# Optimization experiments

Measured on AMD Instinct MI355X. Metric: run time of the kernel, lower is better.

The kernel has to match this reference:

```python
import jax, jax.numpy as jnp
import numpy as np

NUM_DIGIT, DIM_DIGIT, NUM_ROUTINGS = 10, 16, 3
B, NUM_PRIMARY, DIM_PRIMARY = 256, 1152, 8
EPS = 1e-7


def _squash(x, eps=EPS):
    # Faithful to the source: tf.norm with NO axis -> GLOBAL Frobenius norm
    # over the whole tensor (not per-capsule).
    n2 = jnp.sum(jnp.square(x))
    n = jnp.sqrt(n2)
    return (n2 / (n2 + 1.0)) * (x / (n + eps))


def setup_inputs() -> dict:
    key = jax.random.key(0)
    k1, k2 = jax.random.split(key)
    primary_caps = jax.random.normal(k1, (B, NUM_PRIMARY, DIM_PRIMARY), dtype=jnp.float32)
    # glorot_uniform over W [num_digit, num_primary, dim_digit, dim_primary]
    limit = float(np.sqrt(6.0 / (DIM_PRIMARY + DIM_DIGIT)))
    W = jax.random.uniform(k2, (NUM_DIGIT, NUM_PRIMARY, DIM_DIGIT, DIM_PRIMARY),
                           minval=-limit, maxval=limit, dtype=jnp.float32)
    return {"primary_caps": primary_caps, "W": W}


def reference(primary_caps, W):
    # u_hat[b,d,p,i] = sum_j W[d,p,i,j] * primary_caps[b,p,j]
    # (vectorized replacement for tf.map_fn over the batch)
    u_hat = jnp.einsum('dpij,bpj->bdpi', W, primary_caps)  # [B, D, P, dim_digit]

    b = jnp.zeros((u_hat.shape[0], NUM_DIGIT, 1, NUM_PRIMARY), dtype=u_hat.dtype)
    v = None
    for r in range(NUM_ROUTINGS):
        c = jax.nn.softmax(b, axis=1)                      # [B, D, 1, P]
        s = jnp.einsum('bdop,bdpi->bdoi', c, u_hat)        # [B, D, 1, dim_digit]
        v = jnp.transpose(_squash(s), (0, 1, 3, 2))        # [B, D, dim_digit, 1]
        if r < NUM_ROUTINGS - 1:
            agree = jnp.einsum('bdpi,bdio->bdpo', u_hat, v)  # [B, D, P, 1]
            b = b + jnp.transpose(agree, (0, 1, 3, 2))       # [B, D, 1, P]
    return jnp.squeeze(v, axis=-1)  # [B, num_digit, dim_digit]
```

## Files before the change

kernel.cpp:

```cpp
#include <hip/hip_runtime.h>
#include <hip/hip_bf16.h>
#include <stdint.h>

#define B_ 256
#define D_ 10
#define P_ 1152
#define I_ 16
#define J_ 8

#define PG 48
#define NPT 24

__device__ inline uint32_t pack_bf16(float a, float b) {
    uint32_t ua = __float_as_uint(a);
    uint32_t ub = __float_as_uint(b);
    ua = (ua + 0x7fffu + ((ua >> 16) & 1u)) >> 16;
    ub = (ub + 0x7fffu + ((ub >> 16) & 1u)) >> 16;
    return ua | (ub << 16);
}

__global__ __launch_bounds__(256) void k_uhat(
    const float* __restrict__ x, const float* __restrict__ W,
    uint32_t* __restrict__ uhat, float* __restrict__ s_part)
{
    const int bid = blockIdx.x;
    const int bh = bid & 1;
    const int pd = bid >> 1;
    const int d = pd % D_;
    const int pg = pd / D_;
    const int p0 = pg * PG;

    const int tid = threadIdx.x;
    const int ih = tid & 1;
    const int b = bh * 128 + (tid >> 1);

    __shared__ float4 Wl[PG * 32];

    const float4* wg = (const float4*)(W + (size_t)(d * P_ + p0) * 128);
    for (int k = tid; k < PG * 32; k += 256) Wl[k] = wg[k];
    __syncthreads();

    float sacc[8];
    #pragma unroll
    for (int i = 0; i < 8; ++i) sacc[i] = 0.f;

    const float4* xb = (const float4*)(x + ((size_t)b * P_ + p0) * J_);
    uint4* ub = (uint4*)(uhat + ((size_t)(b * D_ + d) * P_ + p0) * 8) + ih;

    float4 xA = xb[0], xB = xb[1];
    for (int pp = 0; pp < PG; ++pp) {
        float4 nA = xA, nB = xB;
        if (pp + 1 < PG) { nA = xb[(pp + 1) * 2]; nB = xb[(pp + 1) * 2 + 1]; }

        const float4* wp = &Wl[pp * 32 + ih * 16];
        float u[8];
        #pragma unroll
        for (int i = 0; i < 8; ++i) {
            const float4 wA = wp[i * 2], wB = wp[i * 2 + 1];
            u[i] = wA.x*xA.x + wA.y*xA.y + wA.z*xA.z + wA.w*xA.w
                 + wB.x*xB.x + wB.y*xB.y + wB.z*xB.z + wB.w*xB.w;
            sacc[i] += u[i];
        }
        uint4 w;
        w.x = pack_bf16(u[0], u[1]); w.y = pack_bf16(u[2], u[3]);
        w.z = pack_bf16(u[4], u[5]); w.w = pack_bf16(u[6], u[7]);
        ub[pp * 2] = w;
        xA = nA; xB = nB;
    }

    float4* sp = (float4*)(s_part + (size_t)pg * (B_ * D_ * I_)
                           + (size_t)b * (D_ * I_) + d * 16 + ih * 8);
    sp[0] = make_float4(sacc[0], sacc[1], sacc[2], sacc[3]);
    sp[1] = make_float4(sacc[4], sacc[5], sacc[6], sacc[7]);
}

__global__ __launch_bounds__(256) void k_sred(const float* __restrict__ s_part,
                                              float* __restrict__ s, float* __restrict__ n2)
{
    const int gid = blockIdx.x * 256 + threadIdx.x;
    float v = 0.f;
    #pragma unroll
    for (int pt = 0; pt < NPT; ++pt) v += s_part[(size_t)pt * (B_ * D_ * I_) + gid];
    v *= 0.1f;
    s[gid] = v;
    float v2 = v * v;
    #pragma unroll
    for (int st = 1; st < 64; st <<= 1) v2 += __shfl_xor(v2, st);
    __shared__ float r4[4];
    const int lane = threadIdx.x & 63, wave = threadIdx.x >> 6;
    if (lane == 0) r4[wave] = v2;
    __syncthreads();
    if (threadIdx.x == 0) atomicAdd(n2, r4[0] + r4[1] + r4[2] + r4[3]);
}

__global__ __launch_bounds__(1024) void k_route(
    const uint32_t* __restrict__ uhat,
    const float* __restrict__ s0, const float* __restrict__ s1,
    const float* __restrict__ n2v, int rnd,
    float* __restrict__ s_out)
{
    const int b = blockIdx.x;
    const int tid = threadIdx.x;

    __shared__ float tls[D_ * I_];
    __shared__ float sw[16][D_ * I_];
    __shared__ float n2l;

    if (tid < D_ * I_) {
        const float n20 = n2v[0];
        const float g0 = (n20 / (n20 + 1.f)) / (sqrtf(n20) + 1e-7f);
        float v = g0 * s0[(size_t)b * D_ * I_ + tid];
        if (rnd == 2) {
            const float n21 = n2v[1];
            const float g1 = (n21 / (n21 + 1.f)) / (sqrtf(n21) + 1e-7f);
            v += g1 * s1[(size_t)b * D_ * I_ + tid];
        }
        tls[tid] = v;
    }
    if (tid == 0) n2l = 0.f;
    __syncthreads();

    const int team = tid >> 3;
    const int tl = tid & 7;
    float sacc[D_][2];
    #pragma unroll
    for (int d = 0; d < D_; ++d) { sacc[d][0] = 0.f; sacc[d][1] = 0.f; }

    for (int k = 0; k < 9; ++k) {
        const int p = team + k * 128;
        const uint32_t* up = uhat + ((size_t)b * D_ * P_ + p) * 8 + tl;
        float u[D_][2];
        float beta[D_];
        #pragma unroll
        for (int d = 0; d < D_; ++d) {
            const uint32_t w = up[(size_t)d * P_ * 8];
            const float u0 = __uint_as_float(w << 16);
            const float u1 = __uint_as_float(w & 0xffff0000u);
            u[d][0] = u0; u[d][1] = u1;
            float bp = u0 * tls[d * I_ + 2 * tl] + u1 * tls[d * I_ + 2 * tl + 1];
            bp += __shfl_xor(bp, 1);
            bp += __shfl_xor(bp, 2);
            bp += __shfl_xor(bp, 4);
            beta[d] = bp;
        }
        float m = beta[0];
        #pragma unroll
        for (int d = 1; d < D_; ++d) m = fmaxf(m, beta[d]);
        float c[D_]; float Z = 0.f;
        #pragma unroll
        for (int d = 0; d < D_; ++d) { c[d] = __expf(beta[d] - m); Z += c[d]; }
        const float rz = 1.f / Z;
        #pragma unroll
        for (int d = 0; d < D_; ++d) {
            const float cd = c[d] * rz;
            sacc[d][0] += cd * u[d][0];
            sacc[d][1] += cd * u[d][1];
        }
    }

    #pragma unroll
    for (int st = 8; st < 64; st <<= 1) {
        #pragma unroll
        for (int d = 0; d < D_; ++d) {
            sacc[d][0] += __shfl_xor(sacc[d][0], st);
            sacc[d][1] += __shfl_xor(sacc[d][1], st);
        }
    }
    const int wave = tid >> 6, lane = tid & 63;
    if (lane < 8) {
        #pragma unroll
        for (int d = 0; d < D_; ++d) {
            sw[wave][d * I_ + 2 * tl]     = sacc[d][0];
            sw[wave][d * I_ + 2 * tl + 1] = sacc[d][1];
        }
    }
    __syncthreads();

    if (tid < D_ * I_) {
        float v = 0.f;
        #pragma unroll
        for (int w2 = 0; w2 < 16; ++w2) v += sw[w2][tid];
        s_out[(size_t)b * D_ * I_ + tid] = v;
        atomicAdd(&n2l, v * v);
    }
    __syncthreads();
    if (tid == 0) atomicAdd((float*)(n2v + rnd), n2l);
}

__global__ void k_out(float* __restrict__ out, const float* __restrict__ n2p)
{
    const int i = blockIdx.x * 256 + threadIdx.x;
    const float n2 = *n2p;
    const float g = (n2 / (n2 + 1.f)) / (sqrtf(n2) + 1e-7f);
    out[i] *= g;
}

extern "C" void kernel_launch(void* const* d_in, const int* in_sizes, int n_in,
                              void* d_out, int out_size, void* d_ws, size_t ws_size,
                              hipStream_t stream)
{
    const float* x = (const float*)d_in[0];
    const float* W = (const float*)d_in[1];
    float* out = (float*)d_out;

    char* ws = (char*)d_ws;
    uint32_t* uhat = (uint32_t*)ws;
    const size_t uhat_bytes = (size_t)B_ * D_ * P_ * I_ * 2;
    float* s_part = (float*)(ws + uhat_bytes);
    float* s0 = s_part + (size_t)NPT * B_ * D_ * I_;
    float* s1 = s0 + B_ * D_ * I_;
    float* n2 = s1 + B_ * D_ * I_;

    hipMemsetAsync(n2, 0, 3 * sizeof(float), stream);

    k_uhat<<<NPT * D_ * 2, 256, 0, stream>>>(x, W, uhat, s_part);
    k_sred<<<(B_ * D_ * I_) / 256, 256, 0, stream>>>(s_part, s0, n2 + 0);
    k_route<<<B_, 1024, 0, stream>>>(uhat, s0, s1, n2, 1, s1);
    k_route<<<B_, 1024, 0, stream>>>(uhat, s0, s1, n2, 2, out);
    k_out<<<(B_ * D_ * I_) / 256, 256, 0, stream>>>(out, n2 + 2);
}
```

Measured before the change: 100.7 us.

## Reshape u_hat storage into slot-interleaved layout and remap uhat kernel threads

Changes the u_hat kernel so each thread computes one pair of output dims for 4 primaries at a time, writing 16-byte packed stores in a new slot-interleaved layout. The W tile in LDS is stored with padding to avoid bank conflicts. Blocks now cover 32 batches each, and block indices are ordered so consecutive blocks share d. The routing kernel's indexing is rewritten to read the new layout. The goals are fewer, wider global stores, better coalescing, and more blocks for occupancy, at the cost of more blocks each reloading W into LDS.

```diff
diff --git a/kernel.cpp b/kernel.cpp
--- a/kernel.cpp
+++ b/kernel.cpp
@@ -10,6 +10,8 @@
 
 #define PG 48
 #define NPT 24
+#define SLOTS 9216
+#define WSP 193
 
 __device__ inline uint32_t pack_bf16(float a, float b) {
     uint32_t ua = __float_as_uint(a);
@@ -24,54 +26,60 @@
     uint32_t* __restrict__ uhat, float* __restrict__ s_part)
 {
     const int bid = blockIdx.x;
-    const int bh = bid & 1;
-    const int pd = bid >> 1;
-    const int d = pd % D_;
-    const int pg = pd / D_;
+    const int g = bid & 7;
+    const int fam = bid >> 3;
+    const int pg = g + 8 * (fam % 3);
+    const int rem = fam / 3;
+    const int d = rem % D_;
+    const int bc = rem / D_;
+
     const int p0 = pg * PG;
-
     const int tid = threadIdx.x;
-    const int ih = tid & 1;
-    const int b = bh * 128 + (tid >> 1);
-
-    __shared__ float4 Wl[PG * 32];
+    const int c = tid & 7;
+    const int b = bc * 32 + (tid >> 3);
+
+    __shared__ float4 Wl[8 * WSP];
 
     const float4* wg = (const float4*)(W + (size_t)(d * P_ + p0) * 128);
-    for (int k = tid; k < PG * 32; k += 256) Wl[k] = wg[k];
-    __syncthreads();
-
-    float sacc[8];
-    #pragma unroll
-    for (int i = 0; i < 8; ++i) sacc[i] = 0.f;
-
+    for (int k = tid; k < PG * 32; k += 256) {
+        const int pl = k >> 5;
+        const int cc = (k >> 2) & 7;
+        const int q = k & 3;
+        Wl[cc * WSP + pl * 4 + q] = wg[k];
+    }
+    __syncthreads();
+
+    float sacc0 = 0.f, sacc1 = 0.f;
     const float4* xb = (const float4*)(x + ((size_t)b * P_ + p0) * J_);
-    uint4* ub = (uint4*)(uhat + ((size_t)(b * D_ + d) * P_ + p0) * 8) + ih;
-
-    float4 xA = xb[0], xB = xb[1];
-    for (int pp = 0; pp < PG; ++pp) {
-        float4 nA = xA, nB = xB;
-        if (pp + 1 < PG) { nA = xb[(pp + 1) * 2]; nB = xb[(pp + 1) * 2 + 1]; }
-
-        const float4* wp = &Wl[pp * 32 + ih * 16];
-        float u[8];
-        #pragma unroll
-        for (int i = 0; i < 8; ++i) {
-            const float4 wA = wp[i * 2], wB = wp[i * 2 + 1];
-            u[i] = wA.x*xA.x + wA.y*xA.y + wA.z*xA.z + wA.w*xA.w
-                 + wB.x*xB.x + wB.y*xB.y + wB.z*xB.z + wB.w*xB.w;
-            sacc[i] += u[i];
-        }
-        uint4 w;
-        w.x = pack_bf16(u[0], u[1]); w.y = pack_bf16(u[2], u[3]);
-        w.z = pack_bf16(u[4], u[5]); w.w = pack_bf16(u[6], u[7]);
-        ub[pp * 2] = w;
-        xA = nA; xB = nB;
-    }
-
-    float4* sp = (float4*)(s_part + (size_t)pg * (B_ * D_ * I_)
-                           + (size_t)b * (D_ * I_) + d * 16 + ih * 8);
-    sp[0] = make_float4(sacc[0], sacc[1], sacc[2], sacc[3]);
-    sp[1] = make_float4(sacc[4], sacc[5], sacc[6], sacc[7]);
+    uint4* ub = (uint4*)uhat + ((size_t)(b * D_ + d) * SLOTS >> 2) + c;
+    const int pqg0 = pg * 12;
+
+    for (int pql = 0; pql < 12; ++pql) {
+        float4 xv[4][2];
+        #pragma unroll
+        for (int p4 = 0; p4 < 4; ++p4) {
+            xv[p4][0] = xb[(pql * 4 + p4) * 2];
+            xv[p4][1] = xb[(pql * 4 + p4) * 2 + 1];
+        }
+        uint32_t wr[4];
+        #pragma unroll
+        for (int p4 = 0; p4 < 4; ++p4) {
+            const float4* wp = &Wl[c * WSP + (pql * 4 + p4) * 4];
+            const float4 wA = wp[0], wB = wp[1], wC = wp[2], wD = wp[3];
+            const float4 xA = xv[p4][0], xB = xv[p4][1];
+            float u0 = wA.x*xA.x + wA.y*xA.y + wA.z*xA.z + wA.w*xA.w
+                     + wB.x*xB.x + wB.y*xB.y + wB.z*xB.z + wB.w*xB.w;
+            float u1 = wC.x*xA.x + wC.y*xA.y + wC.z*xA.z + wC.w*xA.w
+                     + wD.x*xB.x + wD.y*xB.y + wD.z*xB.z + wD.w*xB.w;
+            sacc0 += u0; sacc1 += u1;
+            wr[p4] = pack_bf16(u0, u1);
+        }
+        uint4 w4; w4.x = wr[0]; w4.y = wr[1]; w4.z = wr[2]; w4.w = wr[3];
+        ub[(size_t)(pqg0 + pql) * 8] = w4;
+    }
+
+    float2 o; o.x = sacc0; o.y = sacc1;
+    *(float2*)&s_part[(((size_t)pg * B_ + b) * D_ + d) * I_ + 2 * c] = o;
 }
 
 __global__ __launch_bounds__(256) void k_sred(const float* __restrict__ s_part,
@@ -120,20 +128,25 @@
     if (tid == 0) n2l = 0.f;
     __syncthreads();
 
-    const int team = tid >> 3;
-    const int tl = tid & 7;
+    const int wv = tid >> 6;
+    const int l = tid & 63;
+    const int tb = l >> 3;
+    const int tl = l & 7;
+    const uint32_t* ubase = uhat + (size_t)b * D_ * SLOTS;
+
     float sacc[D_][2];
     #pragma unroll
     for (int d = 0; d < D_; ++d) { sacc[d][0] = 0.f; sacc[d][1] = 0.f; }
 
     for (int k = 0; k < 9; ++k) {
-        const int p = team + k * 128;
-        const uint32_t* up = uhat + ((size_t)b * D_ * P_ + p) * 8 + tl;
+        const int pqb = k * 32 + wv * 2;
+        const int slot = (pqb + (tb >> 2)) * 32 + tl * 4 + (tb & 3);
+        const uint32_t* up = ubase + slot;
         float u[D_][2];
         float beta[D_];
         #pragma unroll
         for (int d = 0; d < D_; ++d) {
-            const uint32_t w = up[(size_t)d * P_ * 8];
+            const uint32_t w = up[(size_t)d * SLOTS];
             const float u0 = __uint_as_float(w << 16);
             const float u1 = __uint_as_float(w & 0xffff0000u);
             u[d][0] = u0; u[d][1] = u1;
@@ -146,13 +159,13 @@
         float m = beta[0];
         #pragma unroll
         for (int d = 1; d < D_; ++d) m = fmaxf(m, beta[d]);
-        float c[D_]; float Z = 0.f;
-        #pragma unroll
-        for (int d = 0; d < D_; ++d) { c[d] = __expf(beta[d] - m); Z += c[d]; }
+        float cc[D_]; float Z = 0.f;
+        #pragma unroll
+        for (int d = 0; d < D_; ++d) { cc[d] = __expf(beta[d] - m); Z += cc[d]; }
         const float rz = 1.f / Z;
         #pragma unroll
         for (int d = 0; d < D_; ++d) {
-            const float cd = c[d] * rz;
+            const float cd = cc[d] * rz;
             sacc[d][0] += cd * u[d][0];
             sacc[d][1] += cd * u[d][1];
         }
@@ -166,12 +179,11 @@
             sacc[d][1] += __shfl_xor(sacc[d][1], st);
         }
     }
-    const int wave = tid >> 6, lane = tid & 63;
-    if (lane < 8) {
-        #pragma unroll
-        for (int d = 0; d < D_; ++d) {
-            sw[wave][d * I_ + 2 * tl]     = sacc[d][0];
-            sw[wave][d * I_ + 2 * tl + 1] = sacc[d][1];
+    if (l < 8) {
+        #pragma unroll
+        for (int d = 0; d < D_; ++d) {
+            sw[wv][d * I_ + 2 * tl]     = sacc[d][0];
+            sw[wv][d * I_ + 2 * tl + 1] = sacc[d][1];
         }
     }
     __syncthreads();
@@ -213,7 +225,7 @@
 
     hipMemsetAsync(n2, 0, 3 * sizeof(float), stream);
 
-    k_uhat<<<NPT * D_ * 2, 256, 0, stream>>>(x, W, uhat, s_part);
+    k_uhat<<<NPT * D_ * 8, 256, 0, stream>>>(x, W, uhat, s_part);
     k_sred<<<(B_ * D_ * I_) / 256, 256, 0, stream>>>(s_part, s0, n2 + 0);
     k_route<<<B_, 1024, 0, stream>>>(uhat, s0, s1, n2, 1, s1);
     k_route<<<B_, 1024, 0, stream>>>(uhat, s0, s1, n2, 2, out);
```

New measurement: 96.68 us. 1.04x faster.

## Recompute u_hat per routing round instead of storing a bf16 u_hat buffer

Applied to the files above, without the earlier changes.

Drops the materialised bf16 u_hat tensor (about 94 MB written once and read twice). Each of the three routing rounds now recomputes u_hat on the fly from x and W, using a single templated kernel that fuses the softmax and weighted sum. Per-block partial sums go through a separate reduction kernel. This trades the HBM traffic of the u_hat buffer for three times the u_hat FLOPs and repeated reads of W and x, which may be served from cache. A side effect is that u_hat stays in fp32 rather than being rounded to bf16.

```diff
diff --git a/kernel.cpp b/kernel.cpp
--- a/kernel.cpp
+++ b/kernel.cpp
@@ -8,81 +8,124 @@
 #define I_ 16
 #define J_ 8
 
-#define PG 48
-#define NPT 24
+#define NPG 16
+#define PRR 72
+#define NB 8
 
-__device__ inline uint32_t pack_bf16(float a, float b) {
-    uint32_t ua = __float_as_uint(a);
-    uint32_t ub = __float_as_uint(b);
-    ua = (ua + 0x7fffu + ((ua >> 16) & 1u)) >> 16;
-    ub = (ub + 0x7fffu + ((ub >> 16) & 1u)) >> 16;
-    return ua | (ub << 16);
-}
-
-__global__ __launch_bounds__(256) void k_uhat(
+template<int RND>
+__global__ __launch_bounds__(512, 2) void k_round(
     const float* __restrict__ x, const float* __restrict__ W,
-    uint32_t* __restrict__ uhat, float* __restrict__ s_part)
+    const float* __restrict__ s0, const float* __restrict__ s1,
+    const float* __restrict__ n2v, float* __restrict__ s_part)
 {
     const int bid = blockIdx.x;
-    const int bh = bid & 1;
-    const int pd = bid >> 1;
-    const int d = pd % D_;
-    const int pg = pd / D_;
-    const int p0 = pg * PG;
+    const int pg = bid & 15;
+    const int bc = bid >> 4;
+    const int tid = threadIdx.x;
+    const int c = tid & 7;
+    const int tm = tid >> 3;
+    const int b_l = tm & 7;
+    const int pidx = tm >> 3;
+    const int b = bc * NB + b_l;
 
-    const int tid = threadIdx.x;
-    const int ih = tid & 1;
-    const int b = bh * 128 + (tid >> 1);
+    __shared__ float lsum[8][NB][D_ * I_];
 
-    __shared__ float4 Wl[PG * 32];
-
-    const float4* wg = (const float4*)(W + (size_t)(d * P_ + p0) * 128);
-    for (int k = tid; k < PG * 32; k += 256) Wl[k] = wg[k];
-    __syncthreads();
-
-    float sacc[8];
-    #pragma unroll
-    for (int i = 0; i < 8; ++i) sacc[i] = 0.f;
-
-    const float4* xb = (const float4*)(x + ((size_t)b * P_ + p0) * J_);
-    uint4* ub = (uint4*)(uhat + ((size_t)(b * D_ + d) * P_ + p0) * 8) + ih;
-
-    float4 xA = xb[0], xB = xb[1];
-    for (int pp = 0; pp < PG; ++pp) {
-        float4 nA = xA, nB = xB;
-        if (pp + 1 < PG) { nA = xb[(pp + 1) * 2]; nB = xb[(pp + 1) * 2 + 1]; }
-
-        const float4* wp = &Wl[pp * 32 + ih * 16];
-        float u[8];
+    float t0[D_], t1[D_];
+    if (RND > 0) {
+        const float n20 = n2v[0];
+        const float g0 = (n20 / (n20 + 1.f)) / (sqrtf(n20) + 1e-7f);
+        const float* sb0 = s0 + (size_t)b * (D_ * I_) + 2 * c;
         #pragma unroll
-        for (int i = 0; i < 8; ++i) {
-            const float4 wA = wp[i * 2], wB = wp[i * 2 + 1];
-            u[i] = wA.x*xA.x + wA.y*xA.y + wA.z*xA.z + wA.w*xA.w
-                 + wB.x*xB.x + wB.y*xB.y + wB.z*xB.z + wB.w*xB.w;
-            sacc[i] += u[i];
+        for (int d = 0; d < D_; ++d) {
+            t0[d] = g0 * sb0[d * 16];
+            t1[d] = g0 * sb0[d * 16 + 1];
         }
-        uint4 w;
-        w.x = pack_bf16(u[0], u[1]); w.y = pack_bf16(u[2], u[3]);
-        w.z = pack_bf16(u[4], u[5]); w.w = pack_bf16(u[6], u[7]);
-        ub[pp * 2] = w;
-        xA = nA; xB = nB;
+        if (RND == 2) {
+            const float n21 = n2v[1];
+            const float g1 = (n21 / (n21 + 1.f)) / (sqrtf(n21) + 1e-7f);
+            const float* sb1 = s1 + (size_t)b * (D_ * I_) + 2 * c;
+            #pragma unroll
+            for (int d = 0; d < D_; ++d) {
+                t0[d] += g1 * sb1[d * 16];
+                t1[d] += g1 * sb1[d * 16 + 1];
+            }
+        }
     }
 
-    float4* sp = (float4*)(s_part + (size_t)pg * (B_ * D_ * I_)
-                           + (size_t)b * (D_ * I_) + d * 16 + ih * 8);
-    sp[0] = make_float4(sacc[0], sacc[1], sacc[2], sacc[3]);
-    sp[1] = make_float4(sacc[4], sacc[5], sacc[6], sacc[7]);
+    float sa0[D_], sa1[D_];
+    #pragma unroll
+    for (int d = 0; d < D_; ++d) { sa0[d] = 0.f; sa1[d] = 0.f; }
+
+    for (int st = 0; st < PRR / 8; ++st) {
+        const int p = pg * PRR + st * 8 + pidx;
+        const float4* xp = (const float4*)(x + ((size_t)b * P_ + p) * J_);
+        const float4 xA = xp[0], xB = xp[1];
+        const float4* wp = (const float4*)(W + ((size_t)p * I_ + 2 * c) * J_);
+
+        float u0[D_], u1[D_], beta[D_];
+        #pragma unroll
+        for (int d = 0; d < D_; ++d) {
+            const float4 wA = wp[0], wB = wp[1], wC = wp[2], wD = wp[3];
+            wp += (size_t)P_ * 32;
+            u0[d] = wA.x*xA.x + wA.y*xA.y + wA.z*xA.z + wA.w*xA.w
+                  + wB.x*xB.x + wB.y*xB.y + wB.z*xB.z + wB.w*xB.w;
+            u1[d] = wC.x*xA.x + wC.y*xA.y + wC.z*xA.z + wC.w*xA.w
+                  + wD.x*xB.x + wD.y*xB.y + wD.z*xB.z + wD.w*xB.w;
+            if (RND > 0) beta[d] = u0[d] * t0[d] + u1[d] * t1[d];
+        }
+
+        if (RND > 0) {
+            #pragma unroll
+            for (int d = 0; d < D_; ++d) {
+                beta[d] += __shfl_xor(beta[d], 1);
+                beta[d] += __shfl_xor(beta[d], 2);
+                beta[d] += __shfl_xor(beta[d], 4);
+            }
+            float m = beta[0];
+            #pragma unroll
+            for (int d = 1; d < D_; ++d) m = fmaxf(m, beta[d]);
+            float Z = 0.f;
+            #pragma unroll
+            for (int d = 0; d < D_; ++d) { beta[d] = __expf(beta[d] - m); Z += beta[d]; }
+            const float rz = 1.f / Z;
+            #pragma unroll
+            for (int d = 0; d < D_; ++d) {
+                const float cd = beta[d] * rz;
+                sa0[d] += cd * u0[d];
+                sa1[d] += cd * u1[d];
+            }
+        } else {
+            #pragma unroll
+            for (int d = 0; d < D_; ++d) { sa0[d] += u0[d]; sa1[d] += u1[d]; }
+        }
+    }
+
+    #pragma unroll
+    for (int d = 0; d < D_; ++d) {
+        lsum[pidx][b_l][d * 16 + 2 * c]     = sa0[d];
+        lsum[pidx][b_l][d * 16 + 2 * c + 1] = sa1[d];
+    }
+    __syncthreads();
+    for (int k = tid; k < NB * D_ * I_; k += 512) {
+        const int bb = k / (D_ * I_);
+        const int di = k - bb * (D_ * I_);
+        float v = 0.f;
+        #pragma unroll
+        for (int q = 0; q < 8; ++q) v += lsum[q][bb][di];
+        s_part[(size_t)pg * (B_ * D_ * I_) + (size_t)(bc * NB + bb) * (D_ * I_) + di] = v;
+    }
 }
 
 __global__ __launch_bounds__(256) void k_sred(const float* __restrict__ s_part,
-                                              float* __restrict__ s, float* __restrict__ n2)
+                                              float* __restrict__ sout,
+                                              float* __restrict__ n2, float scale)
 {
     const int gid = blockIdx.x * 256 + threadIdx.x;
     float v = 0.f;
     #pragma unroll
-    for (int pt = 0; pt < NPT; ++pt) v += s_part[(size_t)pt * (B_ * D_ * I_) + gid];
-    v *= 0.1f;
-    s[gid] = v;
+    for (int pt = 0; pt < NPG; ++pt) v += s_part[(size_t)pt * (B_ * D_ * I_) + gid];
+    v *= scale;
+    sout[gid] = v;
     float v2 = v * v;
     #pragma unroll
     for (int st = 1; st < 64; st <<= 1) v2 += __shfl_xor(v2, st);
@@ -91,100 +134,6 @@
     if (lane == 0) r4[wave] = v2;
     __syncthreads();
     if (threadIdx.x == 0) atomicAdd(n2, r4[0] + r4[1] + r4[2] + r4[3]);
-}
-
-__global__ __launch_bounds__(1024) void k_route(
-    const uint32_t* __restrict__ uhat,
-    const float* __restrict__ s0, const float* __restrict__ s1,
-    const float* __restrict__ n2v, int rnd,
-    float* __restrict__ s_out)
-{
-    const int b = blockIdx.x;
-    const int tid = threadIdx.x;
-
-    __shared__ float tls[D_ * I_];
-    __shared__ float sw[16][D_ * I_];
-    __shared__ float n2l;
-
-    if (tid < D_ * I_) {
-        const float n20 = n2v[0];
-        const float g0 = (n20 / (n20 + 1.f)) / (sqrtf(n20) + 1e-7f);
-        float v = g0 * s0[(size_t)b * D_ * I_ + tid];
-        if (rnd == 2) {
-            const float n21 = n2v[1];
-            const float g1 = (n21 / (n21 + 1.f)) / (sqrtf(n21) + 1e-7f);
-            v += g1 * s1[(size_t)b * D_ * I_ + tid];
-        }
-        tls[tid] = v;
-    }
-    if (tid == 0) n2l = 0.f;
-    __syncthreads();
-
-    const int team = tid >> 3;
-    const int tl = tid & 7;
-    float sacc[D_][2];
-    #pragma unroll
-    for (int d = 0; d < D_; ++d) { sacc[d][0] = 0.f; sacc[d][1] = 0.f; }
-
-    for (int k = 0; k < 9; ++k) {
-        const int p = team + k * 128;
-        const uint32_t* up = uhat + ((size_t)b * D_ * P_ + p) * 8 + tl;
-        float u[D_][2];
-        float beta[D_];
-        #pragma unroll
-        for (int d = 0; d < D_; ++d) {
-            const uint32_t w = up[(size_t)d * P_ * 8];
-            const float u0 = __uint_as_float(w << 16);
-            const float u1 = __uint_as_float(w & 0xffff0000u);
-            u[d][0] = u0; u[d][1] = u1;
-            float bp = u0 * tls[d * I_ + 2 * tl] + u1 * tls[d * I_ + 2 * tl + 1];
-            bp += __shfl_xor(bp, 1);
-            bp += __shfl_xor(bp, 2);
-            bp += __shfl_xor(bp, 4);
-            beta[d] = bp;
-        }
-        float m = beta[0];
-        #pragma unroll
-        for (int d = 1; d < D_; ++d) m = fmaxf(m, beta[d]);
-        float c[D_]; float Z = 0.f;
-        #pragma unroll
-        for (int d = 0; d < D_; ++d) { c[d] = __expf(beta[d] - m); Z += c[d]; }
-        const float rz = 1.f / Z;
-        #pragma unroll
-        for (int d = 0; d < D_; ++d) {
-            const float cd = c[d] * rz;
-            sacc[d][0] += cd * u[d][0];
-            sacc[d][1] += cd * u[d][1];
-        }
-    }
-
-    #pragma unroll
-    for (int st = 8; st < 64; st <<= 1) {
-        #pragma unroll
-        for (int d = 0; d < D_; ++d) {
-            sacc[d][0] += __shfl_xor(sacc[d][0], st);
-            sacc[d][1] += __shfl_xor(sacc[d][1], st);
-        }
-    }
-    const int wave = tid >> 6, lane = tid & 63;
-    if (lane < 8) {
-        #pragma unroll
-        for (int d = 0; d < D_; ++d) {
-            sw[wave][d * I_ + 2 * tl]     = sacc[d][0];
-            sw[wave][d * I_ + 2 * tl + 1] = sacc[d][1];
-        }
-    }
-    __syncthreads();
-
-    if (tid < D_ * I_) {
-        float v = 0.f;
-        #pragma unroll
-        for (int w2 = 0; w2 < 16; ++w2) v += sw[w2][tid];
-        s_out[(size_t)b * D_ * I_ + tid] = v;
-        atomicAdd(&n2l, v * v);
-    }
-    __syncthreads();
-    if (tid == 0) atomicAdd((float*)(n2v + rnd), n2l);
 }
 
 __global__ void k_out(float* __restrict__ out, const float* __restrict__ n2p)
@@ -203,19 +152,21 @@
     const float* W = (const float*)d_in[1];
     float* out = (float*)d_out;
 
-    char* ws = (char*)d_ws;
-    uint32_t* uhat = (uint32_t*)ws;
-    const size_t uhat_bytes = (size_t)B_ * D_ * P_ * I_ * 2;
-    float* s_part = (float*)(ws + uhat_bytes);
-    float* s0 = s_part + (size_t)NPT * B_ * D_ * I_;
+    float* ws = (float*)d_ws;
+    float* s_part = ws;
+    float* s0 = s_part + (size_t)NPG * B_ * D_ * I_;
     float* s1 = s0 + B_ * D_ * I_;
     float* n2 = s1 + B_ * D_ * I_;
 
-    hipMemsetAsync(n2, 0, 3 * sizeof(float), stream);
+    (void)hipMemsetAsync(n2, 0, 3 * sizeof(float), stream);
 
-    k_uhat<<<NPT * D_ * 2, 256, 0, stream>>>(x, W, uhat, s_part);
-    k_sred<<<(B_ * D_ * I_) / 256, 256, 0, stream>>>(s_part, s0, n2 + 0);
-    k_route<<<B_, 1024, 0, stream>>>(uhat, s0, s1, n2, 1, s1);
-    k_route<<<B_, 1024, 0, stream>>>(uhat, s0, s1, n2, 2, out);
+    const int grid = 32 * NPG;
+
+    k_round<0><<<grid, 512, 0, stream>>>(x, W, s0, s1, n2, s_part);
+    k_sred<<<(B_ * D_ * I_) / 256, 256, 0, stream>>>(s_part, s0, n2 + 0, 0.1f);
+    k_round<1><<<grid, 512, 0, stream>>>(x, W, s0, s1, n2, s_part);
+    k_sred<<<(B_ * D_ * I_) / 256, 256, 0, stream>>>(s_part, s1, n2 + 1, 1.0f);
+    k_round<2><<<grid, 512, 0, stream>>>(x, W, s0, s1, n2, s_part);
+    k_sred<<<(B_ * D_ * I_) / 256, 256, 0, stream>>>(s_part, out, n2 + 2, 1.0f);
     k_out<<<(B_ * D_ * I_) / 256, 256, 0, stream>>>(out, n2 + 2);
 }
```

Measured after the change: 275.6 us. +173.7%, slower.
